# Kernel tuning notes

Hardware: AMD Instinct MI355X
Metric: run time of the kernel (lower is better)

Reference implementation:

```python
import jax, jax.numpy as jnp
import numpy as np

E, D, A = 1024, 1024, 512

def setup_inputs() -> dict:
    key = jax.random.key(0)
    ks = jax.random.split(key, 8)
    B, S = 32, 2048
    s_e = 1.0 / np.sqrt(E)
    s_d = 1.0 / np.sqrt(D)
    s_a = 1.0 / np.sqrt(A)
    return {
        "encoder_outputs": jax.random.normal(ks[0], (B, S, E), jnp.float32),
        "decoder_hidden": jax.random.normal(ks[1], (B, D), jnp.float32),
        "We": jax.random.uniform(ks[2], (E, A), jnp.float32, -s_e, s_e),
        "be": jax.random.uniform(ks[3], (A,), jnp.float32, -s_e, s_e),
        "Wd": jax.random.uniform(ks[4], (D, A), jnp.float32, -s_d, s_d),
        "bd": jax.random.uniform(ks[5], (A,), jnp.float32, -s_d, s_d),
        "v_w": jax.random.uniform(ks[6], (A,), jnp.float32, -s_a, s_a),
        "v_b": jax.random.uniform(ks[7], (), jnp.float32, -s_a, s_a),
    }

def reference(encoder_outputs, decoder_hidden, We, be, Wd, bd, v_w, v_b):
    # encoder_energy: [B,S,A]; decoder_energy: [B,1,A]
    enc_e = jnp.einsum('bse,ea->bsa', encoder_outputs, We) + be
    dec_e = (decoder_hidden @ Wd + bd)[:, None, :]
    energy = jnp.tanh(enc_e + dec_e)                     # [B,S,A]
    scores = jnp.einsum('bsa,a->bs', energy, v_w) + v_b  # [B,S]
    attn = jax.nn.softmax(scores, axis=1)                # [B,S]
    context = jnp.einsum('bs,bse->be', attn, encoder_outputs)  # [B,E]
    return context, attn
```

## Files before the change

### kernel.cpp

```cpp
#include <hip/hip_runtime.h>
#include <math.h>

#define E_DIM 1024
#define D_DIM 1024
#define A_DIM 512
#define B_NUM 32
#define S_DIM 2048
#define M_DIM (B_NUM * S_DIM)

typedef unsigned short ushort;
typedef short short8 __attribute__((ext_vector_type(8)));
typedef float f32x4 __attribute__((ext_vector_type(4)));
typedef unsigned short ushort4v __attribute__((ext_vector_type(4)));
typedef unsigned int uint2v __attribute__((ext_vector_type(2)));

typedef const void __attribute__((address_space(1))) cglobal_t;
typedef void __attribute__((address_space(3))) lds_t;

__device__ __forceinline__ void gload_lds16(const void* g, void* l) {
    __builtin_amdgcn_global_load_lds((cglobal_t*)g, (lds_t*)l, 16, 0, 0);
}

__device__ __forceinline__ ushort f2bf(float x) {
    unsigned u = __float_as_uint(x);
    u += 0x7FFF + ((u >> 16) & 1);
    return (ushort)(u >> 16);
}

__device__ __forceinline__ unsigned cvt_pk_bf16(float lo, float hi) {
    unsigned r;
    asm("v_cvt_pk_bf16_f32 %0, %1, %2" : "=v"(r) : "v"(lo), "v"(hi));
    return r;
}

__device__ __forceinline__ float fast_tanh(float x) {
    const float e = __expf(2.0f * x);
    return 1.0f - 2.0f * __builtin_amdgcn_rcpf(e + 1.0f);
}

__global__ __launch_bounds__(256) void k0_dec_energy(
    const float* __restrict__ dh, const float* __restrict__ Wd,
    const float* __restrict__ bd, const float* __restrict__ be,
    float* __restrict__ dec2) {
    __shared__ float sdh[D_DIM];
    const int b = blockIdx.y;
    const int t = threadIdx.x;
    for (int i = t; i < D_DIM; i += 256) sdh[i] = dh[b * D_DIM + i];
    __syncthreads();
    const int a = blockIdx.x * 256 + t;
    float acc = bd[a] + be[a];
#pragma unroll 8
    for (int e = 0; e < D_DIM; ++e) acc += sdh[e] * Wd[(size_t)e * A_DIM + a];
    dec2[b * A_DIM + a] = acc;
}

__global__ __launch_bounds__(256) void k0b_cvt_we(
    const float* __restrict__ We, ushort* __restrict__ Wt) {
    const int n = blockIdx.x;
    const int k0 = threadIdx.x * 4;
    ushort4v v;
#pragma unroll
    for (int j = 0; j < 4; ++j) v[j] = f2bf(We[(size_t)(k0 + j) * A_DIM + n]);
    *reinterpret_cast<ushort4v*>(&Wt[(size_t)n * E_DIM + k0]) = v;
}

#define BM4 128
#define BN4 256
#define NT4 32
#define BUFU4 12288

__global__ __launch_bounds__(256, 2) void k1_fused(
    const float* __restrict__ enc, const ushort* __restrict__ Wt,
    const float* __restrict__ dec2, const float* __restrict__ v_w,
    float* __restrict__ pscores) {
    __shared__ ushort L[2 * BUFU4];

    const int t = threadIdx.x;
    const int l = t & 63;
    const int w = t >> 6;
    const int wm = w >> 1, wn = w & 1;
    const int fr = l & 15;
    const int kg = l >> 4;

    const int o = ((blockIdx.x & 7) << 7) | (blockIdx.x >> 3);
    const int x = o >> 1, ny = o & 1;
    const int row0 = x * BM4;
    const int n0 = ny * BN4;
    const int b = row0 >> 11;

    const int arow = t >> 3;
    const int achk = t & 7;
    const float* AsrcT = enc + (size_t)(row0 + arow) * E_DIM + achk * 4;
    const int aswzc = ((((achk >> 1) ^ ((t >> 4) & 3)) << 4) | ((t & 1) << 3));
    const int awbase = arow * 64 + aswzc;

    const ushort* BsrcQ[4];
#pragma unroll
    for (int q = 0; q < 4; ++q) {
        const int row = q * 64 + w * 16 + (l >> 2);
        const int c = (l & 3) ^ ((row >> 1) & 3);
        BsrcQ[q] = Wt + (size_t)(n0 + row) * E_DIM + c * 8;
    }

    f32x4 acc[4][8];
#pragma unroll
    for (int i = 0; i < 4; ++i)
#pragma unroll
        for (int j = 0; j < 8; ++j) acc[i][j] = (f32x4){0.f, 0.f, 0.f, 0.f};

    float4 paA[4], paB[4];

#define LOADA4(pa, ktv)                                                        \
    {                                                                          \
        _Pragma("unroll") for (int q = 0; q < 4; ++q)                          \
            pa[q] = *reinterpret_cast<const float4*>(                          \
                AsrcT + (size_t)q * 32 * E_DIM + (ktv) * 32);                  \
    }

#define STAGEB4(cb, ktv)                                                       \
    {                                                                          \
        _Pragma("unroll") for (int q = 0; q < 4; ++q)                          \
            gload_lds16(BsrcQ[q] + (ktv) * 32,                                 \
                        L + (cb) * BUFU4 + 4096 + (q * 64 + w * 16) * 32);     \
    }

#define WRITEA4(cb, pa)                                                        \
    {                                                                          \
        _Pragma("unroll") for (int q = 0; q < 4; ++q) {                        \
            uint2v v2;                                                         \
            v2[0] = cvt_pk_bf16(pa[q].x, pa[q].y);                             \
            v2[1] = cvt_pk_bf16(pa[q].z, pa[q].w);                             \
            *reinterpret_cast<uint2v*>(                                        \
                (char*)L + (cb) * 24576 + q * 2048 + awbase) = v2;             \
        }                                                                      \
    }

#define MFMA_BLOCK(cur)                                                        \
    {                                                                          \
        const char* Ab = (const char*)L + (cur) * 24576;                       \
        const char* Bb = Ab + 8192;                                            \
        short8 af[4], bf[8];                                                   \
        _Pragma("unroll") for (int i = 0; i < 4; ++i) {                        \
            const int r = wm * 64 + i * 16 + fr;                               \
            af[i] = *reinterpret_cast<const short8*>(                          \
                Ab + r * 64 + ((kg ^ ((r >> 1) & 3)) << 4));                   \
        }                                                                      \
        _Pragma("unroll") for (int j = 0; j < 8; ++j) {                        \
            const int r = wn * 128 + j * 16 + fr;                              \
            bf[j] = *reinterpret_cast<const short8*>(                          \
                Bb + r * 64 + ((kg ^ ((r >> 1) & 3)) << 4));                   \
        }                                                                      \
        __builtin_amdgcn_s_setprio(1);                                         \
        _Pragma("unroll") for (int i = 0; i < 4; ++i)                          \
            _Pragma("unroll") for (int j = 0; j < 8; ++j)                      \
                acc[i][j] = __builtin_amdgcn_mfma_f32_16x16x32_bf16(           \
                    af[i], bf[j], acc[i][j], 0, 0, 0);                         \
        __builtin_amdgcn_s_setprio(0);                                         \
    }

#define WAITV(n) asm volatile("s_waitcnt vmcnt(" #n ")" ::: "memory")
#define WAITLG() asm volatile("s_waitcnt lgkmcnt(0)" ::: "memory")
#define BARRIER() __builtin_amdgcn_s_barrier()

    LOADA4(paA, 0);
    STAGEB4(0, 0);
    LOADA4(paB, 1);
    WAITV(8);
    WRITEA4(0, paA);
    WAITV(4);
    WAITLG();
    BARRIER();

#define ITER(kt, paW, paL)                                                     \
    {                                                                          \
        const int cur = (kt) & 1;                                              \
        STAGEB4(cur ^ 1, (kt) + 1);                           \
        LOADA4(paL, (kt) + 2);                                \
        MFMA_BLOCK(cur);                                                       \
        WAITV(8);                               \
        WRITEA4(cur ^ 1, paW);                                                 \
        WAITV(4);                       \
        WAITLG();                                                              \
        BARRIER();                                                             \
    }

    for (int kp = 0; kp < 30; kp += 2) {
        ITER(kp, paB, paA);
        ITER(kp + 1, paA, paB);
    }
    {
        STAGEB4(1, 31);
        MFMA_BLOCK(0);
        WAITV(4);
        WRITEA4(1, paB);
        WAITV(0);
        WAITLG();
        BARRIER();
    }
    MFMA_BLOCK(1);

    float rowsum[4][4];
#pragma unroll
    for (int i = 0; i < 4; ++i)
#pragma unroll
        for (int r = 0; r < 4; ++r) rowsum[i][r] = 0.0f;

#pragma unroll
    for (int j = 0; j < 8; ++j) {
        const int ag = n0 + wn * 128 + j * 16 + fr;
        const float bias = dec2[b * A_DIM + ag];
        const float vw = v_w[ag];
#pragma unroll
        for (int i = 0; i < 4; ++i)
#pragma unroll
            for (int r = 0; r < 4; ++r)
                rowsum[i][r] += fast_tanh(acc[i][j][r] + bias) * vw;
    }
#pragma unroll
    for (int m = 1; m < 16; m <<= 1)
#pragma unroll
        for (int i = 0; i < 4; ++i)
#pragma unroll
            for (int r = 0; r < 4; ++r)
                rowsum[i][r] += __shfl_xor(rowsum[i][r], m, 64);

    __syncthreads();
    float* red = reinterpret_cast<float*>(L);
    if (fr == 0) {
#pragma unroll
        for (int i = 0; i < 4; ++i)
#pragma unroll
            for (int r = 0; r < 4; ++r)
                red[(wm * 64 + i * 16 + kg * 4 + r) * 2 + wn] = rowsum[i][r];
    }
    __syncthreads();
    if (t < BM4)
        pscores[(size_t)(row0 + t) * 2 + ny] = red[t * 2] + red[t * 2 + 1];
}

__global__ __launch_bounds__(256) void k2_softmax(
    const float* __restrict__ pscores, const float* __restrict__ v_b,
    float* __restrict__ attn_out, int W) {
    __shared__ float sc[S_DIM];
    __shared__ float red[8];
    const int b = blockIdx.x;
    const int t = threadIdx.x;
    const int wave = t >> 6, lane = t & 63;
    const float vb = v_b[0];

    float lmax = -1e30f;
    for (int s = t; s < S_DIM; s += 256) {
        float v = vb;
        for (int c = 0; c < W; ++c) v += pscores[(size_t)(b * S_DIM + s) * W + c];
        sc[s] = v;
        lmax = fmaxf(lmax, v);
    }
#pragma unroll
    for (int off = 32; off > 0; off >>= 1) lmax = fmaxf(lmax, __shfl_down(lmax, off, 64));
    if (lane == 0) red[wave] = lmax;
    __syncthreads();
    const float bmax = fmaxf(fmaxf(red[0], red[1]), fmaxf(red[2], red[3]));

    float lsum = 0.0f;
    for (int s = t; s < S_DIM; s += 256) {
        const float e = expf(sc[s] - bmax);
        sc[s] = e;
        lsum += e;
    }
#pragma unroll
    for (int off = 32; off > 0; off >>= 1) lsum += __shfl_down(lsum, off, 64);
    if (lane == 0) red[4 + wave] = lsum;
    __syncthreads();
    const float inv = 1.0f / (red[4] + red[5] + red[6] + red[7]);
    for (int s = t; s < S_DIM; s += 256) attn_out[b * S_DIM + s] = sc[s] * inv;
}

#define SC_CHUNK 128
#define N_SC (S_DIM / SC_CHUNK)
__global__ __launch_bounds__(256) void k3_ctx_partial(
    const float* __restrict__ enc, const float* __restrict__ attn,
    float* __restrict__ pctx) {
    const int b = blockIdx.y;
    const int scb = blockIdx.x;
    const int t = threadIdx.x;
    const int s0 = scb * SC_CHUNK;
    float4 acc = {0.0f, 0.0f, 0.0f, 0.0f};
    const float4* encv =
        reinterpret_cast<const float4*>(enc + (size_t)(b * S_DIM + s0) * E_DIM);
#pragma unroll 4
    for (int s = 0; s < SC_CHUNK; ++s) {
        const float w = attn[b * S_DIM + s0 + s];
        const float4 v = encv[(size_t)s * (E_DIM / 4) + t];
        acc.x += w * v.x;
        acc.y += w * v.y;
        acc.z += w * v.z;
        acc.w += w * v.w;
    }
    *reinterpret_cast<float4*>(&pctx[(size_t)(b * N_SC + scb) * E_DIM + t * 4]) = acc;
}

__global__ __launch_bounds__(256) void k4_ctx_reduce(
    const float* __restrict__ pctx, float* __restrict__ ctx) {
    const int b = blockIdx.x;
    const int t = threadIdx.x;
    float4 acc = {0.0f, 0.0f, 0.0f, 0.0f};
#pragma unroll
    for (int s = 0; s < N_SC; ++s) {
        const float4 v = *reinterpret_cast<const float4*>(
            &pctx[(size_t)(b * N_SC + s) * E_DIM + t * 4]);
        acc.x += v.x;
        acc.y += v.y;
        acc.z += v.z;
        acc.w += v.w;
    }
    *reinterpret_cast<float4*>(&ctx[(size_t)b * E_DIM + t * 4]) = acc;
}

extern "C" void kernel_launch(void* const* d_in, const int* in_sizes, int n_in,
                              void* d_out, int out_size, void* d_ws, size_t ws_size,
                              hipStream_t stream) {
    (void)in_sizes; (void)n_in; (void)out_size; (void)ws_size;
    const float* enc = (const float*)d_in[0];
    const float* dh  = (const float*)d_in[1];
    const float* We  = (const float*)d_in[2];
    const float* be  = (const float*)d_in[3];
    const float* Wd  = (const float*)d_in[4];
    const float* bd  = (const float*)d_in[5];
    const float* vw  = (const float*)d_in[6];
    const float* vb  = (const float*)d_in[7];

    float* out = (float*)d_out;
    float* ctx_out = out;
    float* attn_out = out + B_NUM * E_DIM;

    float* ws = (float*)d_ws;
    float* dec2    = ws;
    float* pscores = ws + 16384;
    float* pctx    = ws + 16384 + 131072;
    ushort* Wt     = (ushort*)(ws + 16384 + 131072 + 524288);

    k0_dec_energy<<<dim3(2, 32), 256, 0, stream>>>(dh, Wd, bd, be, dec2);
    k0b_cvt_we<<<dim3(A_DIM), 256, 0, stream>>>(We, Wt);
    k1_fused<<<dim3((M_DIM / BM4) * (A_DIM / BN4)), 256, 0, stream>>>(
        enc, Wt, dec2, vw, pscores);
    k2_softmax<<<dim3(B_NUM), 256, 0, stream>>>(pscores, vb, attn_out, 2);
    k3_ctx_partial<<<dim3(N_SC, B_NUM), 256, 0, stream>>>(enc, attn_out, pctx);
    k4_ctx_reduce<<<dim3(B_NUM), 256, 0, stream>>>(pctx, ctx_out);
}
```

Before: 206.5 us.

## Emit bf16 copy of encoder outputs in GEMM and read it for context

The fused score GEMM now writes a bf16 copy of the encoder tile it already loaded and converted, but only from the ny==0 blocks. A new bf16 context kernel reads that copy instead of the fp32 encoder, halving the bytes the context pass reads. In exchange the GEMM writes an extra 128MB, the context is computed from bf16-rounded values, and the path depends on the workspace being large enough.

Result: slower. 237.7 us (+15.1%).

```diff
diff --git a/kernel.cpp b/kernel.cpp
--- a/kernel.cpp
+++ b/kernel.cpp
@@ -72,7 +72,7 @@
 __global__ __launch_bounds__(256, 2) void k1_fused(
     const float* __restrict__ enc, const ushort* __restrict__ Wt,
     const float* __restrict__ dec2, const float* __restrict__ v_w,
-    float* __restrict__ pscores) {
+    float* __restrict__ pscores, ushort* __restrict__ ebf) {
     __shared__ ushort L[2 * BUFU4];
 
     const int t = threadIdx.x;
@@ -87,12 +87,16 @@
     const int row0 = x * BM4;
     const int n0 = ny * BN4;
     const int b = row0 >> 11;
+    const bool doStore = (ebf != nullptr) && (ny == 0);
 
     const int arow = t >> 3;
     const int achk = t & 7;
     const float* AsrcT = enc + (size_t)(row0 + arow) * E_DIM + achk * 4;
     const int aswzc = ((((achk >> 1) ^ ((t >> 4) & 3)) << 4) | ((t & 1) << 3));
     const int awbase = arow * 64 + aswzc;
+    ushort* EbT = (ebf != nullptr)
+                      ? ebf + (size_t)(row0 + arow) * E_DIM + achk * 4
+                      : nullptr;
 
     const ushort* BsrcQ[4];
 #pragma unroll
@@ -132,6 +136,17 @@
             v2[1] = cvt_pk_bf16(pa[q].z, pa[q].w);                             \
             *reinterpret_cast<uint2v*>(                                        \
                 (char*)L + (cb) * 24576 + q * 2048 + awbase) = v2;             \
+        }                                                                      \
+    }
+
+#define STOREA4(pa, ktv)                                                       \
+    if (doStore) {                                                             \
+        _Pragma("unroll") for (int q = 0; q < 4; ++q) {                        \
+            uint2v v2;                                                         \
+            v2[0] = cvt_pk_bf16(pa[q].x, pa[q].y);                             \
+            v2[1] = cvt_pk_bf16(pa[q].z, pa[q].w);                             \
+            *reinterpret_cast<uint2v*>(                                        \
+                EbT + (size_t)q * 32 * E_DIM + (ktv) * 32) = v2;               \
         }                                                                      \
     }
 
@@ -168,6 +183,7 @@
     WAITV(8);
     WRITEA4(0, paA);
     WAITV(4);
+    STOREA4(paA, 0);
     WAITLG();
     BARRIER();
 
@@ -175,11 +191,12 @@
     {                                                                          \
         const int cur = (kt) & 1;                                              \
         STAGEB4(cur ^ 1, (kt) + 1);                           \
-        LOADA4(paL, (kt) + 2);                                \
+        LOADA4(paL, (kt) + 2);                          \
         MFMA_BLOCK(cur);                                                       \
-        WAITV(8);                               \
+        WAITV(8);                                  \
         WRITEA4(cur ^ 1, paW);                                                 \
-        WAITV(4);                       \
+        WAITV(4);                             \
+        STOREA4(paW, (kt) + 1);                                 \
         WAITLG();                                                              \
         BARRIER();                                                             \
     }
@@ -194,6 +211,7 @@
         WAITV(4);
         WRITEA4(1, paB);
         WAITV(0);
+        STOREA4(paB, 31);
         WAITLG();
         BARRIER();
     }
@@ -277,6 +295,33 @@
 
 #define SC_CHUNK 128
 #define N_SC (S_DIM / SC_CHUNK)
+__global__ __launch_bounds__(128) void k3_ctx_bf16(
+    const ushort* __restrict__ ebf, const float* __restrict__ attn,
+    float* __restrict__ pctx) {
+    const int b = blockIdx.y;
+    const int scb = blockIdx.x;
+    const int t = threadIdx.x;
+    const int s0 = scb * SC_CHUNK;
+    float acc[8];
+#pragma unroll
+    for (int j = 0; j < 8; ++j) acc[j] = 0.0f;
+    const ushort* base = ebf + (size_t)(b * S_DIM + s0) * E_DIM + t * 8;
+#pragma unroll 4
+    for (int s = 0; s < SC_CHUNK; ++s) {
+        const float wgt = attn[b * S_DIM + s0 + s];
+        const int4 v = *reinterpret_cast<const int4*>(base + (size_t)s * E_DIM);
+        const unsigned* u = reinterpret_cast<const unsigned*>(&v);
+#pragma unroll
+        for (int j = 0; j < 4; ++j) {
+            acc[2 * j] += wgt * __uint_as_float(u[j] << 16);
+            acc[2 * j + 1] += wgt * __uint_as_float(u[j] & 0xffff0000u);
+        }
+    }
+    float* dst = &pctx[(size_t)(b * N_SC + scb) * E_DIM + t * 8];
+    *reinterpret_cast<float4*>(dst) = make_float4(acc[0], acc[1], acc[2], acc[3]);
+    *reinterpret_cast<float4*>(dst + 4) = make_float4(acc[4], acc[5], acc[6], acc[7]);
+}
+
 __global__ __launch_bounds__(256) void k3_ctx_partial(
     const float* __restrict__ enc, const float* __restrict__ attn,
     float* __restrict__ pctx) {
@@ -319,7 +364,7 @@
 extern "C" void kernel_launch(void* const* d_in, const int* in_sizes, int n_in,
                               void* d_out, int out_size, void* d_ws, size_t ws_size,
                               hipStream_t stream) {
-    (void)in_sizes; (void)n_in; (void)out_size; (void)ws_size;
+    (void)in_sizes; (void)n_in; (void)out_size;
     const float* enc = (const float*)d_in[0];
     const float* dh  = (const float*)d_in[1];
     const float* We  = (const float*)d_in[2];
@@ -338,12 +383,19 @@
     float* pscores = ws + 16384;
     float* pctx    = ws + 16384 + 131072;
     ushort* Wt     = (ushort*)(ws + 16384 + 131072 + 524288);
+    const size_t fixed_bytes = (16384ull + 131072 + 524288) * 4 + 1048576;
+    const size_t NEED = fixed_bytes + (size_t)M_DIM * E_DIM * 2;
+    ushort* ebf = (ws_size >= NEED) ? (ushort*)((char*)d_ws + fixed_bytes) : nullptr;
 
     k0_dec_energy<<<dim3(2, 32), 256, 0, stream>>>(dh, Wd, bd, be, dec2);
     k0b_cvt_we<<<dim3(A_DIM), 256, 0, stream>>>(We, Wt);
     k1_fused<<<dim3((M_DIM / BM4) * (A_DIM / BN4)), 256, 0, stream>>>(
-        enc, Wt, dec2, vw, pscores);
+        enc, Wt, dec2, vw, pscores, ebf);
     k2_softmax<<<dim3(B_NUM), 256, 0, stream>>>(pscores, vb, attn_out, 2);
-    k3_ctx_partial<<<dim3(N_SC, B_NUM), 256, 0, stream>>>(enc, attn_out, pctx);
+    if (ebf != nullptr) {
+        k3_ctx_bf16<<<dim3(N_SC, B_NUM), 128, 0, stream>>>(ebf, attn_out, pctx);
+    } else {
+        k3_ctx_partial<<<dim3(N_SC, B_NUM), 256, 0, stream>>>(enc, attn_out, pctx);
+    }
     k4_ctx_reduce<<<dim3(B_NUM), 256, 0, stream>>>(pctx, ctx_out);
 }
```
